# Kernel optimization log

Hardware: AMD Instinct MI355X
Metric: run time of the kernel (lower is better)

## Reference

```python
import jax, jax.numpy as jnp
import numpy as np

N = 100000
D = 128
E = 1600000


def setup_inputs() -> dict:
    key = jax.random.key(0)
    k1, k2, k3, k4 = jax.random.split(key, 4)
    x = jax.random.normal(k1, (N, D), dtype=jnp.float32)
    edge_index = jax.random.randint(k2, (2, E), 0, N, dtype=jnp.int64)
    edge_weight = jax.random.uniform(k3, (E,), dtype=jnp.float32)
    x0 = jax.random.normal(k4, (N, D), dtype=jnp.float32)
    return {
        "t": jnp.zeros((), dtype=jnp.float32),
        "x": x,
        "edge_index": edge_index,
        "edge_weight": edge_weight,
        "x0": x0,
        "alpha_train": jnp.zeros((), dtype=jnp.float32),
        "beta_train": jnp.zeros((), dtype=jnp.float32),
        "source_train": jnp.zeros((), dtype=jnp.float32),
    }


def reference(t, x, edge_index, edge_weight, x0, alpha_train, beta_train, source_train):
    # sigmoid-gated diffusion/reaction coefficients
    alpha = jax.nn.sigmoid(alpha_train) * 0.1
    beta = jax.nn.sigmoid(beta_train) * 0.1
    # sparse A @ x: out[row] += w * x[col]  (torch_sparse.spmm convention)
    row, col = edge_index[0], edge_index[1]
    msgs = x[col] * edge_weight[:, None]            # [E, D]
    ax = jax.ops.segment_sum(msgs, row, num_segments=N)  # [N, D]
    diffusion = ax - x
    reaction = -(x - 1.0) * x
    f = alpha * diffusion + beta * reaction
    source_term = jnp.clip(source_train * x0, -1.0, 1.0)
    return f + source_term * 0.1
```

## Files before the change

### kernel.cpp

```cpp
#include <hip/hip_runtime.h>
#include <math.h>


#define D_FEAT 128
#define RPB 128
#define NB_MAX 800
#define SORT_CAP 2560
#define EPB 8192
#define MAXBLK 256

__device__ __forceinline__ float sigmoid_f(float v) {
    return 1.0f / (1.0f + __expf(-v));
}

__device__ __forceinline__ unsigned bf16rn(float f) {
    unsigned u = __float_as_uint(f);
    return (u + 0x7FFFu + ((u >> 16) & 1u)) >> 16;
}

__global__ __launch_bounds__(256) void cvt_kernel(const float* __restrict__ x,
                                                  unsigned short* __restrict__ xb,
                                                  int n8, int* __restrict__ cursors) {
    int i = blockIdx.x * 256 + threadIdx.x;
    if (blockIdx.x == 0 && threadIdx.x == 0) { cursors[0] = 0; cursors[1] = 0; }
    if (!xb || i >= n8) return;
    const float4* x4 = (const float4*)x;
    float4 f0 = x4[(size_t)i * 2];
    float4 f1 = x4[(size_t)i * 2 + 1];
    uint4 o;
    o.x = bf16rn(f0.x) | (bf16rn(f0.y) << 16);
    o.y = bf16rn(f0.z) | (bf16rn(f0.w) << 16);
    o.z = bf16rn(f1.x) | (bf16rn(f1.y) << 16);
    o.w = bf16rn(f1.z) | (bf16rn(f1.w) << 16);
    ((uint4*)xb)[i] = o;
}

__global__ __launch_bounds__(256) void place_kernel(const int* __restrict__ rows,
                                                    const int* __restrict__ cols,
                                                    const float* __restrict__ w,
                                                    const float* __restrict__ alpha_p,
                                                    int* __restrict__ arenaCur,
                                                    int2* __restrict__ arena,
                                                    unsigned* __restrict__ dir,
                                                    int* __restrict__ blkBase,
                                                    int E, int NB) {
    __shared__ int2 sbuf[EPB];
    __shared__ int hist[NB_MAX];
    __shared__ int lexcl[NB_MAX];
    __shared__ int scanb[256];
    __shared__ int gbase_sh;
    int t = threadIdx.x;
    int blk = blockIdx.x;
    int base = blk * EPB;
    for (int i = t; i < NB; i += 256) hist[i] = 0;
    __syncthreads();

#pragma unroll
    for (int k = 0; k < EPB / 256; ++k) {
        int e = base + k * 256 + t;
        if (e < E) atomicAdd(&hist[rows[e] >> 7], 1);
    }
    __syncthreads();

    const int CHK = 4;
    int loc[CHK];
    int run = 0;
#pragma unroll
    for (int k = 0; k < CHK; ++k) {
        int idx = t * CHK + k;
        int v = (idx < NB) ? hist[idx] : 0;
        loc[k] = run; run += v;
    }
    scanb[t] = run;
    __syncthreads();
    for (int d = 1; d < 256; d <<= 1) {
        int tv = (t >= d) ? scanb[t - d] : 0;
        __syncthreads();
        scanb[t] += tv;
        __syncthreads();
    }
    int excl = scanb[t] - run;
    int total = scanb[255];
#pragma unroll
    for (int k = 0; k < CHK; ++k) {
        int idx = t * CHK + k;
        if (idx < NB) lexcl[idx] = excl + loc[k];
    }
    if (t == 0) gbase_sh = atomicAdd(arenaCur, total);
    __syncthreads();
    for (int i = t; i < NB; i += 256) hist[i] = lexcl[i];
    __syncthreads();
    int gbase = gbase_sh;
    const float alpha = sigmoid_f(alpha_p[0]) * 0.1f;

#pragma unroll
    for (int k = 0; k < EPB / 256; ++k) {
        int e = base + k * 256 + t;
        if (e >= E) continue;
        int r = rows[e];
        int bkt = r >> 7;
        int rl  = r & 127;
        int pos = atomicAdd(&hist[bkt], 1);
        sbuf[pos] = make_int2((rl << 17) | cols[e], __float_as_int(w[e] * alpha));
    }
    __syncthreads();

    for (int i = t; i < total; i += 256) arena[gbase + i] = sbuf[i];
    for (int b = t; b < NB; b += 256) {
        int le  = lexcl[b];
        int len = ((b + 1 < NB) ? lexcl[b + 1] : total) - le;
        dir[(size_t)blk * NB + b] = ((unsigned)le << 14) | (unsigned)len;
    }
    if (t == 0) blkBase[blk] = gbase;
}

__global__ __launch_bounds__(256) void sort_kernel(const int2* __restrict__ arena,
                                                   const unsigned* __restrict__ dir,
                                                   const int* __restrict__ blkBase,
                                                   int nBlk,
                                                   int2* __restrict__ col_w,
                                                   int* __restrict__ outCur,
                                                   int* __restrict__ off,
                                                   int* __restrict__ bstart2,
                                                   int N, int NB) {
    __shared__ int2 sbuf[SORT_CAP];
    __shared__ int2 obuf[SORT_CAP];
    __shared__ int pre[MAXBLK + 1];
    __shared__ int abase[MAXBLK];
    __shared__ int scanb[256];
    __shared__ int hist[RPB];
    __shared__ int hscan[RPB];
    __shared__ int cursor[RPB];
    __shared__ int gb_sh;
    int b = blockIdx.x;
    int t = threadIdx.x;

    int len = 0;
    if (t < nBlk) {
        unsigned d = dir[(size_t)t * NB + b];
        len = (int)(d & 0x3FFFu);
        abase[t] = blkBase[t] + (int)(d >> 14);
    }
    scanb[t] = len;
    __syncthreads();
    for (int d = 1; d < 256; d <<= 1) {
        int tv = (t >= d) ? scanb[t - d] : 0;
        __syncthreads();
        scanb[t] += tv;
        __syncthreads();
    }
    if (t < nBlk) pre[t] = scanb[t] - len;
    if (t == 0) {
        int total = scanb[nBlk - 1];
        pre[nBlk] = total;
        gb_sh = atomicAdd(outCur, total);
    }
    if (t < RPB) hist[t] = 0;
    __syncthreads();
    int cntb  = pre[nBlk];
    int gbase = gb_sh;
    bool fast = (cntb <= SORT_CAP);

    for (int i = t; i < cntb; i += 256) {
        int lo = 0, hi = nBlk;
        while (hi - lo > 1) { int m = (lo + hi) >> 1; if (pre[m] <= i) lo = m; else hi = m; }
        int2 rec = arena[abase[lo] + (i - pre[lo])];
        if (fast) sbuf[i] = rec;
        atomicAdd(&hist[rec.x >> 17], 1);
    }
    __syncthreads();

    int v = 0;
    if (t < RPB) { v = hist[t]; hscan[t] = v; }
    __syncthreads();
    for (int d = 1; d < RPB; d <<= 1) {
        int tv = (t >= d && t < RPB) ? hscan[t - d] : 0;
        __syncthreads();
        if (t < RPB) hscan[t] += tv;
        __syncthreads();
    }
    if (t < RPB) {
        int incl = hscan[t];
        int excl = incl - v;
        int row = b * RPB + t;
        if (row < N) off[row] = gbase + incl;
        cursor[t] = fast ? excl : (gbase + excl);
    }
    if (t == 0) bstart2[b] = gbase;
    __syncthreads();

    if (fast) {
        for (int i = t; i < cntb; i += 256) {
            int2 r = sbuf[i];
            int rl = r.x >> 17;
            int pos = atomicAdd(&cursor[rl], 1);
            obuf[pos] = make_int2(r.x & 0x1FFFF, r.y);
        }
        __syncthreads();
        for (int i = t; i < cntb; i += 256)
            col_w[gbase + i] = obuf[i];
    } else {
        for (int i = t; i < cntb; i += 256) {
            int lo = 0, hi = nBlk;
            while (hi - lo > 1) { int m = (lo + hi) >> 1; if (pre[m] <= i) lo = m; else hi = m; }
            int2 r = arena[abase[lo] + (i - pre[lo])];
            int rl = r.x >> 17;
            int pos = atomicAdd(&cursor[rl], 1);
            col_w[pos] = make_int2(r.x & 0x1FFFF, r.y);
        }
    }
}

__global__ void gather_bf16_kernel(const float* __restrict__ x,
                                   const unsigned short* __restrict__ xb,
                                   const float* __restrict__ x0,
                                   const int* __restrict__ off,
                                   const int* __restrict__ bstart2,
                                   const int2* __restrict__ col_w,
                                   const float* __restrict__ alpha_p,
                                   const float* __restrict__ beta_p,
                                   const float* __restrict__ src_p,
                                   float* __restrict__ out, int N) {
    const float alpha = sigmoid_f(alpha_p[0]) * 0.1f;
    const float beta  = sigmoid_f(beta_p[0]) * 0.1f;
    const float src   = src_p[0];

    int gtid = blockIdx.x * blockDim.x + threadIdx.x;
    int row  = gtid >> 6;
    if (row >= N) return;
    int lane  = threadIdx.x & 63;
    int half  = lane >> 5;
    int flane = lane & 31;

    int start = ((row & 127) == 0) ? bstart2[row >> 7] : off[row - 1];
    int end   = off[row];

    const uint2* xb2 = (const uint2*)xb;
    float4 a0 = make_float4(0.f, 0.f, 0.f, 0.f);
    float4 a1 = make_float4(0.f, 0.f, 0.f, 0.f);
    float4 a2 = make_float4(0.f, 0.f, 0.f, 0.f);
    float4 a3 = make_float4(0.f, 0.f, 0.f, 0.f);

#define BF16_FMA(ACC, V, W)                                                    \
    {                                                                          \
        float b0 = __uint_as_float((V).x << 16);                               \
        float b1 = __uint_as_float((V).x & 0xFFFF0000u);                       \
        float b2 = __uint_as_float((V).y << 16);                               \
        float b3 = __uint_as_float((V).y & 0xFFFF0000u);                       \
        ACC.x += (W) * b0; ACC.y += (W) * b1;                                  \
        ACC.z += (W) * b2; ACC.w += (W) * b3;                                  \
    }

    int j = start + half;
    for (; j + 6 < end; j += 8) {
        int2 cw0 = col_w[j];
        int2 cw1 = col_w[j + 2];
        int2 cw2 = col_w[j + 4];
        int2 cw3 = col_w[j + 6];
        uint2 v0 = xb2[(size_t)cw0.x * 32 + flane];
        uint2 v1 = xb2[(size_t)cw1.x * 32 + flane];
        uint2 v2 = xb2[(size_t)cw2.x * 32 + flane];
        uint2 v3 = xb2[(size_t)cw3.x * 32 + flane];
        float w0 = __int_as_float(cw0.y);
        float w1 = __int_as_float(cw1.y);
        float w2 = __int_as_float(cw2.y);
        float w3 = __int_as_float(cw3.y);
        BF16_FMA(a0, v0, w0);
        BF16_FMA(a1, v1, w1);
        BF16_FMA(a2, v2, w2);
        BF16_FMA(a3, v3, w3);
    }
    for (; j + 2 < end; j += 4) {
        int2 cw0 = col_w[j];
        int2 cw1 = col_w[j + 2];
        uint2 v0 = xb2[(size_t)cw0.x * 32 + flane];
        uint2 v1 = xb2[(size_t)cw1.x * 32 + flane];
        float w0 = __int_as_float(cw0.y);
        float w1 = __int_as_float(cw1.y);
        BF16_FMA(a0, v0, w0);
        BF16_FMA(a1, v1, w1);
    }
    if (j < end) {
        int2 cw = col_w[j];
        uint2 v = xb2[(size_t)cw.x * 32 + flane];
        float wv = __int_as_float(cw.y);
        BF16_FMA(a0, v, wv);
    }
#undef BF16_FMA

    float4 acc;
    acc.x = (a0.x + a1.x) + (a2.x + a3.x);
    acc.y = (a0.y + a1.y) + (a2.y + a3.y);
    acc.z = (a0.z + a1.z) + (a2.z + a3.z);
    acc.w = (a0.w + a1.w) + (a2.w + a3.w);

    acc.x += __shfl_xor(acc.x, 32);
    acc.y += __shfl_xor(acc.y, 32);
    acc.z += __shfl_xor(acc.z, 32);
    acc.w += __shfl_xor(acc.w, 32);

    if (half == 0) {
        long long base = (long long)row * 32 + flane;
        float4 xv = ((const float4*)x)[base];
        float4 x0v = make_float4(0.f, 0.f, 0.f, 0.f);
        if (src != 0.0f)
            x0v = ((const float4*)x0)[base];
        float xs[4]  = {xv.x, xv.y, xv.z, xv.w};
        float zs[4]  = {x0v.x, x0v.y, x0v.z, x0v.w};
        float as[4]  = {acc.x, acc.y, acc.z, acc.w};
        float os[4];
#pragma unroll
        for (int k = 0; k < 4; ++k) {
            float reaction = -(xs[k] - 1.0f) * xs[k];
            float st = fminf(fmaxf(src * zs[k], -1.0f), 1.0f);
            os[k] = as[k] - alpha * xs[k] + beta * reaction + st * 0.1f;
        }
        ((float4*)out)[base] = make_float4(os[0], os[1], os[2], os[3]);
    }
}

__global__ void gather_f32_kernel(const float* __restrict__ x,
                                  const float* __restrict__ x0,
                                  const int* __restrict__ off,
                                  const int* __restrict__ bstart2,
                                  const int2* __restrict__ col_w,
                                  const float* __restrict__ alpha_p,
                                  const float* __restrict__ beta_p,
                                  const float* __restrict__ src_p,
                                  float* __restrict__ out, int N) {
    const float alpha = sigmoid_f(alpha_p[0]) * 0.1f;
    const float beta  = sigmoid_f(beta_p[0]) * 0.1f;
    const float src   = src_p[0];

    int gtid = blockIdx.x * blockDim.x + threadIdx.x;
    int row  = gtid >> 6;
    if (row >= N) return;
    int lane  = threadIdx.x & 63;
    int half  = lane >> 5;
    int flane = lane & 31;

    int start = ((row & 127) == 0) ? bstart2[row >> 7] : off[row - 1];
    int end   = off[row];

    const float4* x4 = (const float4*)x;
    float4 a0 = make_float4(0.f, 0.f, 0.f, 0.f);
    float4 a1 = make_float4(0.f, 0.f, 0.f, 0.f);

    int j = start + half;
    for (; j + 2 < end; j += 4) {
        int2 cw0 = col_w[j];
        int2 cw1 = col_w[j + 2];
        float4 v0 = x4[(long long)cw0.x * 32 + flane];
        float4 v1 = x4[(long long)cw1.x * 32 + flane];
        float w0 = __int_as_float(cw0.y);
        float w1 = __int_as_float(cw1.y);
        a0.x += w0 * v0.x; a0.y += w0 * v0.y; a0.z += w0 * v0.z; a0.w += w0 * v0.w;
        a1.x += w1 * v1.x; a1.y += w1 * v1.y; a1.z += w1 * v1.z; a1.w += w1 * v1.w;
    }
    if (j < end) {
        int2 cw = col_w[j];
        float4 v = x4[(long long)cw.x * 32 + flane];
        float wv = __int_as_float(cw.y);
        a0.x += wv * v.x; a0.y += wv * v.y; a0.z += wv * v.z; a0.w += wv * v.w;
    }
    float4 acc;
    acc.x = a0.x + a1.x; acc.y = a0.y + a1.y;
    acc.z = a0.z + a1.z; acc.w = a0.w + a1.w;

    acc.x += __shfl_xor(acc.x, 32);
    acc.y += __shfl_xor(acc.y, 32);
    acc.z += __shfl_xor(acc.z, 32);
    acc.w += __shfl_xor(acc.w, 32);

    if (half == 0) {
        long long base = (long long)row * 32 + flane;
        float4 xv  = x4[base];
        float4 x0v = make_float4(0.f, 0.f, 0.f, 0.f);
        if (src != 0.0f)
            x0v = ((const float4*)x0)[base];
        float xs[4]  = {xv.x, xv.y, xv.z, xv.w};
        float zs[4]  = {x0v.x, x0v.y, x0v.z, x0v.w};
        float as[4]  = {acc.x, acc.y, acc.z, acc.w};
        float os[4];
#pragma unroll
        for (int k = 0; k < 4; ++k) {
            float reaction = -(xs[k] - 1.0f) * xs[k];
            float st = fminf(fmaxf(src * zs[k], -1.0f), 1.0f);
            os[k] = as[k] - alpha * xs[k] + beta * reaction + st * 0.1f;
        }
        ((float4*)out)[base] = make_float4(os[0], os[1], os[2], os[3]);
    }
}

extern "C" void kernel_launch(void* const* d_in, const int* in_sizes, int n_in,
                              void* d_out, int out_size, void* d_ws, size_t ws_size,
                              hipStream_t stream) {
    const float* x   = (const float*)d_in[1];
    const int*   ei  = (const int*)d_in[2];
    const float* ew  = (const float*)d_in[3];
    const float* x0  = (const float*)d_in[4];
    const float* alp = (const float*)d_in[5];
    const float* bet = (const float*)d_in[6];
    const float* src = (const float*)d_in[7];
    float* out = (float*)d_out;

    const int E = in_sizes[3];
    const int N = out_size / D_FEAT;
    const int* rows = ei;
    const int* cols = ei + E;

    const int NB   = (N + RPB - 1) / RPB;
    const int nBlk = (E + EPB - 1) / EPB;

    char* ws = (char*)d_ws;
    char* ws_end = (char*)d_ws + ws_size;
    int*  off     = (int*)ws;  ws += ((size_t)N * 4 + 15) & ~15ull;
    int*  bstart2 = (int*)ws;  ws += ((size_t)NB * 4 + 15) & ~15ull;
    int2* col_w   = (int2*)ws; ws += ((size_t)E * 8 + 15) & ~15ull;

    char* ob = (char*)d_out;
    int2*     arena   = (int2*)ob;       ob += ((size_t)E * 8 + 15) & ~15ull;
    unsigned* dir     = (unsigned*)ob;   ob += ((size_t)nBlk * NB * 4 + 15) & ~15ull;
    int*      blkBase = (int*)ob;        ob += ((size_t)nBlk * 4 + 15) & ~15ull;
    int*      cursors = (int*)ob;        ob += 16;
    bool out_scratch_ok = (ob <= (char*)d_out + out_size);
    if (!out_scratch_ok) {
        arena   = (int2*)ws;     ws += ((size_t)E * 8 + 15) & ~15ull;
        dir     = (unsigned*)ws; ws += ((size_t)nBlk * NB * 4 + 15) & ~15ull;
        blkBase = (int*)ws;      ws += ((size_t)nBlk * 4 + 15) & ~15ull;
        cursors = (int*)ws;      ws += 16;
    }

    unsigned short* xb = nullptr;
    size_t xb_bytes = ((size_t)N * D_FEAT * 2 + 15) & ~15ull;
    if (ws + xb_bytes <= ws_end) {
        xb = (unsigned short*)ws;  ws += xb_bytes;
    }

    {
        int n8 = (N * D_FEAT) / 8;
        int grid = xb ? (n8 + 255) / 256 : 1;
        cvt_kernel<<<grid, 256, 0, stream>>>(x, xb, n8, cursors);
    }
    place_kernel<<<nBlk, 256, 0, stream>>>(rows, cols, ew, alp,
                                           &cursors[0], arena, dir, blkBase, E, NB);
    sort_kernel<<<NB, 256, 0, stream>>>(arena, dir, blkBase, nBlk,
                                        col_w, &cursors[1], off, bstart2, N, NB);
    {
        long long threads = (long long)N * 64;
        int grid = (int)((threads + 255) / 256);
        if (xb)
            gather_bf16_kernel<<<grid, 256, 0, stream>>>(x, xb, x0, off, bstart2,
                                                         col_w, alp, bet, src, out, N);
        else
            gather_f32_kernel<<<grid, 256, 0, stream>>>(x, x0, off, bstart2,
                                                        col_w, alp, bet, src, out, N);
    }
}
```

Measured before the change: 315.2 us.

## Pack CSR edges into 32-bit col/bf16-weight words and scatter directly from registers

The sorted edge array now stores each edge as one 32-bit word: a 17-bit column index plus a 15-bit bf16 weight with the sign bit dropped. This halves the edge-stream bytes read by the gather kernels and written by the sort. The place kernel no longer stages its 8192-entry int2 buffer in LDS. It batches row, column and weight loads into registers and scatters straight to the arena, which frees a large LDS allocation for occupancy at the cost of less coalesced arena writes. Weights lose precision to bf16, and the packing relies on non-negative weights and N below 2^17.

```diff
diff --git a/kernel.cpp b/kernel.cpp
--- a/kernel.cpp
+++ b/kernel.cpp
@@ -44,7 +44,6 @@
                                                     unsigned* __restrict__ dir,
                                                     int* __restrict__ blkBase,
                                                     int E, int NB) {
-    __shared__ int2 sbuf[EPB];
     __shared__ int hist[NB_MAX];
     __shared__ int lexcl[NB_MAX];
     __shared__ int scanb[256];
@@ -55,11 +54,15 @@
     for (int i = t; i < NB; i += 256) hist[i] = 0;
     __syncthreads();
 
-#pragma unroll
-    for (int k = 0; k < EPB / 256; ++k) {
+    int rr[32];
+#pragma unroll
+    for (int k = 0; k < 32; ++k) {
         int e = base + k * 256 + t;
-        if (e < E) atomicAdd(&hist[rows[e] >> 7], 1);
-    }
+        rr[k] = (e < E) ? rows[e] : -1;
+    }
+#pragma unroll
+    for (int k = 0; k < 32; ++k)
+        if (rr[k] >= 0) atomicAdd(&hist[rr[k] >> 7], 1);
     __syncthreads();
 
     const int CHK = 4;
@@ -94,18 +97,27 @@
     const float alpha = sigmoid_f(alpha_p[0]) * 0.1f;
 
 #pragma unroll
-    for (int k = 0; k < EPB / 256; ++k) {
-        int e = base + k * 256 + t;
-        if (e >= E) continue;
-        int r = rows[e];
-        int bkt = r >> 7;
-        int rl  = r & 127;
-        int pos = atomicAdd(&hist[bkt], 1);
-        sbuf[pos] = make_int2((rl << 17) | cols[e], __float_as_int(w[e] * alpha));
-    }
-    __syncthreads();
-
-    for (int i = t; i < total; i += 256) arena[gbase + i] = sbuf[i];
+    for (int g = 0; g < 4; ++g) {
+        int   cc[8];
+        float wwv[8];
+#pragma unroll
+        for (int k = 0; k < 8; ++k) {
+            int e = base + (g * 8 + k) * 256 + t;
+            cc[k]  = (e < E) ? cols[e] : 0;
+            wwv[k] = (e < E) ? w[e]    : 0.0f;
+        }
+#pragma unroll
+        for (int k = 0; k < 8; ++k) {
+            int r = rr[g * 8 + k];
+            if (r < 0) continue;
+            int bkt = r >> 7;
+            int pos = atomicAdd(&hist[bkt], 1);
+            arena[gbase + pos] = make_int2(((r & 127) << 17) | cc[k],
+                                           __float_as_int(wwv[k] * alpha));
+        }
+    }
+    __syncthreads();
+
     for (int b = t; b < NB; b += 256) {
         int le  = lexcl[b];
         int len = ((b + 1 < NB) ? lexcl[b + 1] : total) - le;
@@ -118,13 +130,13 @@
                                                    const unsigned* __restrict__ dir,
                                                    const int* __restrict__ blkBase,
                                                    int nBlk,
-                                                   int2* __restrict__ col_w,
+                                                   unsigned* __restrict__ col_w,
                                                    int* __restrict__ outCur,
                                                    int* __restrict__ off,
                                                    int* __restrict__ bstart2,
                                                    int N, int NB) {
     __shared__ int2 sbuf[SORT_CAP];
-    __shared__ int2 obuf[SORT_CAP];
+    __shared__ unsigned obuf[SORT_CAP];
     __shared__ int pre[MAXBLK + 1];
     __shared__ int abase[MAXBLK];
     __shared__ int scanb[256];
@@ -194,7 +206,8 @@
             int2 r = sbuf[i];
             int rl = r.x >> 17;
             int pos = atomicAdd(&cursor[rl], 1);
-            obuf[pos] = make_int2(r.x & 0x1FFFF, r.y);
+            unsigned wb = bf16rn(__int_as_float(r.y)) & 0x7FFFu;
+            obuf[pos] = (wb << 17) | (unsigned)(r.x & 0x1FFFF);
         }
         __syncthreads();
         for (int i = t; i < cntb; i += 256)
@@ -206,7 +219,8 @@
             int2 r = arena[abase[lo] + (i - pre[lo])];
             int rl = r.x >> 17;
             int pos = atomicAdd(&cursor[rl], 1);
-            col_w[pos] = make_int2(r.x & 0x1FFFF, r.y);
+            unsigned wb = bf16rn(__int_as_float(r.y)) & 0x7FFFu;
+            col_w[pos] = (wb << 17) | (unsigned)(r.x & 0x1FFFF);
         }
     }
 }
@@ -216,7 +230,7 @@
                                    const float* __restrict__ x0,
                                    const int* __restrict__ off,
                                    const int* __restrict__ bstart2,
-                                   const int2* __restrict__ col_w,
+                                   const unsigned* __restrict__ col_w,
                                    const float* __restrict__ alpha_p,
                                    const float* __restrict__ beta_p,
                                    const float* __restrict__ src_p,
@@ -250,43 +264,45 @@
         ACC.x += (W) * b0; ACC.y += (W) * b1;                                  \
         ACC.z += (W) * b2; ACC.w += (W) * b3;                                  \
     }
+#define UNPACK_W(P) __uint_as_float(((P) >> 17) << 16)
 
     int j = start + half;
     for (; j + 6 < end; j += 8) {
-        int2 cw0 = col_w[j];
-        int2 cw1 = col_w[j + 2];
-        int2 cw2 = col_w[j + 4];
-        int2 cw3 = col_w[j + 6];
-        uint2 v0 = xb2[(size_t)cw0.x * 32 + flane];
-        uint2 v1 = xb2[(size_t)cw1.x * 32 + flane];
-        uint2 v2 = xb2[(size_t)cw2.x * 32 + flane];
-        uint2 v3 = xb2[(size_t)cw3.x * 32 + flane];
-        float w0 = __int_as_float(cw0.y);
-        float w1 = __int_as_float(cw1.y);
-        float w2 = __int_as_float(cw2.y);
-        float w3 = __int_as_float(cw3.y);
+        unsigned p0 = col_w[j];
+        unsigned p1 = col_w[j + 2];
+        unsigned p2 = col_w[j + 4];
+        unsigned p3 = col_w[j + 6];
+        uint2 v0 = xb2[(size_t)(p0 & 0x1FFFF) * 32 + flane];
+        uint2 v1 = xb2[(size_t)(p1 & 0x1FFFF) * 32 + flane];
+        uint2 v2 = xb2[(size_t)(p2 & 0x1FFFF) * 32 + flane];
+        uint2 v3 = xb2[(size_t)(p3 & 0x1FFFF) * 32 + flane];
+        float w0 = UNPACK_W(p0);
+        float w1 = UNPACK_W(p1);
+        float w2 = UNPACK_W(p2);
+        float w3 = UNPACK_W(p3);
         BF16_FMA(a0, v0, w0);
         BF16_FMA(a1, v1, w1);
         BF16_FMA(a2, v2, w2);
         BF16_FMA(a3, v3, w3);
     }
     for (; j + 2 < end; j += 4) {
-        int2 cw0 = col_w[j];
-        int2 cw1 = col_w[j + 2];
-        uint2 v0 = xb2[(size_t)cw0.x * 32 + flane];
-        uint2 v1 = xb2[(size_t)cw1.x * 32 + flane];
-        float w0 = __int_as_float(cw0.y);
-        float w1 = __int_as_float(cw1.y);
+        unsigned p0 = col_w[j];
+        unsigned p1 = col_w[j + 2];
+        uint2 v0 = xb2[(size_t)(p0 & 0x1FFFF) * 32 + flane];
+        uint2 v1 = xb2[(size_t)(p1 & 0x1FFFF) * 32 + flane];
+        float w0 = UNPACK_W(p0);
+        float w1 = UNPACK_W(p1);
         BF16_FMA(a0, v0, w0);
         BF16_FMA(a1, v1, w1);
     }
     if (j < end) {
-        int2 cw = col_w[j];
-        uint2 v = xb2[(size_t)cw.x * 32 + flane];
-        float wv = __int_as_float(cw.y);
+        unsigned p = col_w[j];
+        uint2 v = xb2[(size_t)(p & 0x1FFFF) * 32 + flane];
+        float wv = UNPACK_W(p);
         BF16_FMA(a0, v, wv);
     }
 #undef BF16_FMA
+#undef UNPACK_W
 
     float4 acc;
     acc.x = (a0.x + a1.x) + (a2.x + a3.x);
@@ -323,7 +339,7 @@
                                   const float* __restrict__ x0,
                                   const int* __restrict__ off,
                                   const int* __restrict__ bstart2,
-                                  const int2* __restrict__ col_w,
+                                  const unsigned* __restrict__ col_w,
                                   const float* __restrict__ alpha_p,
                                   const float* __restrict__ beta_p,
                                   const float* __restrict__ src_p,
@@ -348,19 +364,19 @@
 
     int j = start + half;
     for (; j + 2 < end; j += 4) {
-        int2 cw0 = col_w[j];
-        int2 cw1 = col_w[j + 2];
-        float4 v0 = x4[(long long)cw0.x * 32 + flane];
-        float4 v1 = x4[(long long)cw1.x * 32 + flane];
-        float w0 = __int_as_float(cw0.y);
-        float w1 = __int_as_float(cw1.y);
+        unsigned p0 = col_w[j];
+        unsigned p1 = col_w[j + 2];
+        float4 v0 = x4[(long long)(p0 & 0x1FFFF) * 32 + flane];
+        float4 v1 = x4[(long long)(p1 & 0x1FFFF) * 32 + flane];
+        float w0 = __uint_as_float((p0 >> 17) << 16);
+        float w1 = __uint_as_float((p1 >> 17) << 16);
         a0.x += w0 * v0.x; a0.y += w0 * v0.y; a0.z += w0 * v0.z; a0.w += w0 * v0.w;
         a1.x += w1 * v1.x; a1.y += w1 * v1.y; a1.z += w1 * v1.z; a1.w += w1 * v1.w;
     }
     if (j < end) {
-        int2 cw = col_w[j];
-        float4 v = x4[(long long)cw.x * 32 + flane];
-        float wv = __int_as_float(cw.y);
+        unsigned p = col_w[j];
+        float4 v = x4[(long long)(p & 0x1FFFF) * 32 + flane];
+        float wv = __uint_as_float((p >> 17) << 16);
         a0.x += wv * v.x; a0.y += wv * v.y; a0.z += wv * v.z; a0.w += wv * v.w;
     }
     float4 acc;
@@ -414,17 +430,16 @@
 
     char* ws = (char*)d_ws;
     char* ws_end = (char*)d_ws + ws_size;
-    int*  off     = (int*)ws;  ws += ((size_t)N * 4 + 15) & ~15ull;
-    int*  bstart2 = (int*)ws;  ws += ((size_t)NB * 4 + 15) & ~15ull;
-    int2* col_w   = (int2*)ws; ws += ((size_t)E * 8 + 15) & ~15ull;
+    int*      off     = (int*)ws;      ws += ((size_t)N * 4 + 15) & ~15ull;
+    int*      bstart2 = (int*)ws;      ws += ((size_t)NB * 4 + 15) & ~15ull;
+    unsigned* col_w   = (unsigned*)ws; ws += ((size_t)E * 4 + 15) & ~15ull;
 
     char* ob = (char*)d_out;
     int2*     arena   = (int2*)ob;       ob += ((size_t)E * 8 + 15) & ~15ull;
     unsigned* dir     = (unsigned*)ob;   ob += ((size_t)nBlk * NB * 4 + 15) & ~15ull;
     int*      blkBase = (int*)ob;        ob += ((size_t)nBlk * 4 + 15) & ~15ull;
     int*      cursors = (int*)ob;        ob += 16;
-    bool out_scratch_ok = (ob <= (char*)d_out + out_size);
-    if (!out_scratch_ok) {
+    if (ob > (char*)d_out + out_size) {
         arena   = (int2*)ws;     ws += ((size_t)E * 8 + 15) & ~15ull;
         dir     = (unsigned*)ws; ws += ((size_t)nBlk * NB * 4 + 15) & ~15ull;
         blkBase = (int*)ws;      ws += ((size_t)nBlk * 4 + 15) & ~15ull;
```

Result: faster. 283.6 us (-10.0%).
